# Kernel tuning notes

Measured on AMD Instinct MI355X. Metric: run time of the kernel, lower is better.

## Reference

```python
import jax, jax.numpy as jnp
import numpy as np

BS, SL, N_AGENTS, OBS_DIM, STATE_DIM, N_EDGES, HID = 32, 512, 32, 96, 1024, 64, 256


def _hgcn(w_line, x, H):
    # x: [B, n, 1]; H: [B, n, E]. Faithful to torch HGCN:
    # A = D^{-1/2} H |W| B^{-1} H^T D^{-1/2}, with D, B built from detached H/|W|,
    # inf entries (from 0^{-1} / 0^{-0.5}) zeroed. Diagonal matmuls are implicit scalings.
    w_abs = jnp.abs(w_line)
    Hd = jax.lax.stop_gradient(H)
    d = jnp.einsum('bne,e->bn', Hd, jax.lax.stop_gradient(w_abs))  # [B, n]
    d_is = jnp.where(d > 0, jax.lax.rsqrt(jnp.where(d > 0, d, 1.0)), 0.0)
    b = jnp.sum(Hd, axis=-2)  # [B, E]
    b_inv = jnp.where(b > 0, 1.0 / jnp.where(b > 0, b, 1.0), 0.0)
    t = d_is[..., None] * x                       # D^{-1/2} x
    s = jnp.einsum('bne,bnk->bek', H, t)          # H^T (...)
    s = s * (w_abs[None, :] * b_inv)[..., None]   # |W| B^{-1} (diagonals commute)
    y = jnp.einsum('bne,bek->bnk', H, s)          # H (...)
    return d_is[..., None] * y                    # D^{-1/2} (...)


def _mlp(x, w1, b1, w2, b2):
    return jax.nn.relu(x @ w1 + b1) @ w2 + b2


def setup_inputs() -> dict:
    key = jax.random.key(0)
    ks = jax.random.split(key, 24)
    f = jax.random.normal
    inp = {
        'agent_qs': f(ks[0], (BS, SL, N_AGENTS), jnp.float32),
        'states': f(ks[1], (BS, SL, STATE_DIM), jnp.float32),
        'indiv_us': f(ks[2], (BS, SL, N_AGENTS, OBS_DIM), jnp.float32),
        'edge_W': f(ks[3], (OBS_DIM, N_EDGES), jnp.float32) * 0.1,
        'edge_b': f(ks[4], (N_EDGES,), jnp.float32) * 0.1,
        'wline1': 1.0 + 0.1 * f(ks[5], (N_EDGES,), jnp.float32),
        'wline2': 1.0 + 0.1 * f(ks[6], (N_EDGES,), jnp.float32),
    }
    names = ['hw1', 'hc1', 'hw', 'hc']
    outs = [N_AGENTS, N_AGENTS, N_AGENTS, 1]
    for i, (nm, od) in enumerate(zip(names, outs)):
        inp[nm + '_w1'] = f(ks[7 + 4 * i], (STATE_DIM, HID), jnp.float32) * 0.05
        inp[nm + '_b1'] = f(ks[8 + 4 * i], (HID,), jnp.float32) * 0.05
        inp[nm + '_w2'] = f(ks[9 + 4 * i], (HID, od), jnp.float32) * 0.05
        inp[nm + '_b2'] = f(ks[10 + 4 * i], (od,), jnp.float32) * 0.05
    return inp


def reference(agent_qs, states, indiv_us, edge_W, edge_b, wline1, wline2,
              hw1_w1, hw1_b1, hw1_w2, hw1_b2, hc1_w1, hc1_b1, hc1_w2, hc1_b2,
              hw_w1, hw_b1, hw_w2, hw_b2, hc_w1, hc_b1, hc_w2, hc_b2):
    bs, sl, n = agent_qs.shape
    q = agent_qs.reshape(-1, n)                               # [B, n]
    u = indiv_us.reshape(-1, n, indiv_us.shape[-1])           # [B, n, obs]
    s = states.reshape(-1, states.shape[-1])                  # [B, state_dim]
    H = jax.nn.relu(u @ edge_W + edge_b)                      # hyper_edge_net -> [B, n, E]
    x = q[..., None]                                          # node_features [B, n, 1]
    qs_tot = _hgcn(wline2, _hgcn(wline1, x, H), H)[..., 0]    # two stacked HGCN encoders
    w1 = jnp.abs(_mlp(s, hw1_w1, hw1_b1, hw1_w2, hw1_b2))
    c1 = _mlp(s, hc1_w1, hc1_b1, hc1_w2, hc1_b2)
    qt = jax.nn.elu(qs_tot * w1 + c1)
    w = jnp.abs(_mlp(s, hw_w1, hw_b1, hw_w2, hw_b2))
    c = _mlp(s, hc_w1, hc_b1, hc_w2, hc_b2)[..., 0]
    q_tot = jnp.sum(qt * w, axis=-1) + c
    return q_tot.reshape(bs, sl, 1)
```

## Files before the change

kernel.cpp:

```cpp
#include <hip/hip_runtime.h>
#include <cstdint>

typedef _Float16 f16;
typedef _Float16 f16x2 __attribute__((ext_vector_type(2)));
typedef _Float16 f16x4 __attribute__((ext_vector_type(4)));
typedef _Float16 f16x8 __attribute__((ext_vector_type(8)));
typedef float f32x4 __attribute__((ext_vector_type(4)));

#define AS1U const __attribute__((address_space(1))) unsigned int
#define AS3U __attribute__((address_space(3))) unsigned int

__device__ __forceinline__ void gload_lds16(const void* g, void* l) {
    __builtin_amdgcn_global_load_lds((AS1U*)g, (AS3U*)l, 16, 0, 0);
}

#define WSYNC() asm volatile("s_waitcnt lgkmcnt(0)" ::: "memory")
#define CFENCE() asm volatile("" ::: "memory")

#define BATCH 16384
#define NAG   32
#define OBS   96
#define SDIM  1024
#define NE    64
#define HIDN  256
#define NH    1024

#define NB_ST 1024
#define NB_PW 256
#define NB_SM 101
#define NB_FRONT (NB_ST + NB_PW + NB_SM)

__global__ __launch_bounds__(256) void k_front(
    const float* __restrict__ states,
    const float* __restrict__ w1a, const float* __restrict__ w1b,
    const float* __restrict__ w1c, const float* __restrict__ w1d,
    const float* __restrict__ b1a, const float* __restrict__ b1b,
    const float* __restrict__ b1c, const float* __restrict__ b1d,
    const float* __restrict__ w2a, const float* __restrict__ w2b,
    const float* __restrict__ w2c, const float* __restrict__ w2d,
    f16* __restrict__ states16, f16* __restrict__ W1t, float* __restrict__ b1cat,
    f16* __restrict__ W2t, f16* __restrict__ hcw2) {
    __shared__ float tile[64 * 65];
    const int tid = threadIdx.x;
    int bid = blockIdx.x;

    if (bid < NB_ST) {
        int i = bid * 256 + tid;
        const int n4 = BATCH * SDIM / 4;
        const int stride = NB_ST * 256;
        for (; i < n4; i += stride) {
            float4 v = ((const float4*)states)[i];
            f16x4 h = { (f16)v.x, (f16)v.y, (f16)v.z, (f16)v.w };
            ((f16x4*)states16)[i] = h;
        }
        return;
    }
    bid -= NB_ST;
    if (bid < NB_PW) {
        int mlp = bid >> 6, rem = bid & 63, kt = rem >> 2, ct = rem & 3;
        const float* src = (mlp == 0) ? w1a : (mlp == 1) ? w1b : (mlp == 2) ? w1c : w1d;
        int k0 = kt * 64, c0 = ct * 64;
        for (int i = tid; i < 4096; i += 256) {
            int kk = i >> 6, cc = i & 63;
            tile[kk * 65 + cc] = src[(size_t)(k0 + kk) * 256 + c0 + cc];
        }
        __syncthreads();
        for (int i = tid; i < 4096; i += 256) {
            int cc = i >> 6, kk = i & 63;
            W1t[(size_t)(mlp * 256 + c0 + cc) * 1024 + k0 + kk] = (f16)tile[kk * 65 + cc];
        }
        return;
    }
    bid -= NB_PW;
    {
        int i = bid * 256 + tid;
        if (i < 24576) {
            int mp = i >> 13, rem = i & 8191, oo = rem >> 8, kk = rem & 255;
            const float* src = (mp == 0) ? w2a : (mp == 1) ? w2b : w2c;
            W2t[i] = (f16)src[kk * 32 + oo];
        } else if (i < 24832) {
            int k = i - 24576;
            hcw2[k] = (f16)w2d[k];
        } else if (i < 25856) {
            int n = i - 24832;
            int mlp = n >> 8, c = n & 255;
            const float* bsrc = (mlp == 0) ? b1a : (mlp == 1) ? b1b : (mlp == 2) ? b1c : b1d;
            b1cat[n] = bsrc[c];
        }
    }
}

__global__ __launch_bounds__(512) void k_gemm(
    const f16* __restrict__ A, const f16* __restrict__ B,
    const float* __restrict__ b1cat, const f16* __restrict__ W2t,
    const f16* __restrict__ hcw2, float* __restrict__ Pp) {
    __shared__ __align__(16) char smem[131072];
    f16* Asb = (f16*)smem;
    f16* Bsb = (f16*)(smem + 65536);
    f16* Ts  = (f16*)smem;

    const int tid = threadIdx.x;
    const int w = tid >> 6, l = tid & 63;
    const int lm = l & 15, lk = l >> 4;
    const int wm = w >> 2, wn = w & 3;
    const int p = blockIdx.x;
    const int xcd = p & 7, s = p >> 3;
    const int mt = xcd * 8 + (s >> 2);
    const int nt = s & 3;
    const int m0 = mt * 256, n0 = nt * 256;
    const int c0 = w * 4;
    const int srow = l >> 3;
    const int gchunk = (l & 7) ^ srow;

    float bj[4];
    #pragma unroll
    for (int j = 0; j < 4; j++) bj[j] = b1cat[n0 + wn * 64 + j * 16 + lm];

    f32x4 acc[8][4];
    #pragma unroll
    for (int i = 0; i < 8; i++)
        #pragma unroll
        for (int j = 0; j < 4; j++) acc[i][j] = (f32x4){0.f, 0.f, 0.f, 0.f};

#define STAGE(KT, BI)                                                                     \
    {                                                                                     \
        f16* Ad = Asb + (BI) * 16384;                                                     \
        f16* Bd = Bsb + (BI) * 16384;                                                     \
        _Pragma("unroll")                                                                 \
        for (int i_ = 0; i_ < 4; i_++) {                                                  \
            int cc = c0 + i_;                                                             \
            gload_lds16(&A[(size_t)(m0 + cc * 8 + srow) * 1024 + (KT) * 64 + gchunk * 8], \
                        &Ad[cc * 512]);                                                   \
            gload_lds16(&B[(size_t)(n0 + cc * 8 + srow) * 1024 + (KT) * 64 + gchunk * 8], \
                        &Bd[cc * 512]);                                                   \
        }                                                                                 \
    }

    STAGE(0, 0);
    STAGE(1, 1);

    for (int kt = 0; kt < 16; kt++) {
        if (kt < 15) { asm volatile("s_waitcnt vmcnt(8)" ::: "memory"); }
        else         { asm volatile("s_waitcnt vmcnt(0)" ::: "memory"); }
        CFENCE(); __builtin_amdgcn_s_barrier(); CFENCE();

        const f16* As_ = Asb + (kt & 1) * 16384;
        const f16* Bs_ = Bsb + (kt & 1) * 16384;
        __builtin_amdgcn_s_setprio(1);
        #pragma unroll
        for (int ks = 0; ks < 2; ks++) {
            const int sw = (((ks * 4 + lk) ^ (lm & 7)) << 3);
            f16x8 af[8], bf[4];
            #pragma unroll
            for (int i = 0; i < 8; i++)
                af[i] = *(const f16x8*)&As_[(wm * 128 + i * 16 + lm) * 64 + sw];
            #pragma unroll
            for (int j = 0; j < 4; j++)
                bf[j] = *(const f16x8*)&Bs_[(wn * 64 + j * 16 + lm) * 64 + sw];
            #pragma unroll
            for (int i = 0; i < 8; i++)
                #pragma unroll
                for (int j = 0; j < 4; j++)
                    acc[i][j] = __builtin_amdgcn_mfma_f32_16x16x32_f16(af[i], bf[j], acc[i][j], 0, 0, 0);
        }
        __builtin_amdgcn_s_setprio(0);

        CFENCE(); __builtin_amdgcn_s_barrier(); CFENCE();
        if (kt < 14) STAGE(kt + 2, kt & 1);
    }
#undef STAGE

    const int mlp = nt;
    #pragma unroll
    for (int pass = 0; pass < 2; pass++) {
        if (wm == pass) {
            #pragma unroll
            for (int i = 0; i < 8; i++)
                #pragma unroll
                for (int r = 0; r < 4; r++) {
                    int rl = i * 16 + lk * 4 + r;
                    #pragma unroll
                    for (int j = 0; j < 4; j++) {
                        float v = acc[i][j][r] + bj[j];
                        Ts[rl * 264 + wn * 64 + j * 16 + lm] = (f16)(v > 0.f ? v : 0.f);
                    }
                }
        }
        __syncthreads();
        const int grow = m0 + pass * 128 + w * 16;
        if (mlp < 3) {
            const f16* wb = W2t + mlp * 8192;
            f32x4 acc2[2];
            acc2[0] = (f32x4){0, 0, 0, 0}; acc2[1] = (f32x4){0, 0, 0, 0};
            #pragma unroll
            for (int ks = 0; ks < 8; ks++) {
                f16x8 a  = *(const f16x8*)&Ts[(w * 16 + lm) * 264 + ks * 32 + lk * 8];
                f16x8 b0 = *(const f16x8*)&wb[lm * 256 + ks * 32 + lk * 8];
                f16x8 b1 = *(const f16x8*)&wb[(16 + lm) * 256 + ks * 32 + lk * 8];
                acc2[0] = __builtin_amdgcn_mfma_f32_16x16x32_f16(a, b0, acc2[0], 0, 0, 0);
                acc2[1] = __builtin_amdgcn_mfma_f32_16x16x32_f16(a, b1, acc2[1], 0, 0, 0);
            }
            #pragma unroll
            for (int j2 = 0; j2 < 2; j2++)
                #pragma unroll
                for (int r = 0; r < 4; r++)
                    Pp[(size_t)(grow + lk * 4 + r) * 104 + mlp * 32 + j2 * 16 + lm] = acc2[j2][r];
        } else {
            f32x4 acc2 = (f32x4){0, 0, 0, 0};
            #pragma unroll
            for (int ks = 0; ks < 8; ks++) {
                f16x8 a = *(const f16x8*)&Ts[(w * 16 + lm) * 264 + ks * 32 + lk * 8];
                f16x8 bz = (f16x8){0, 0, 0, 0, 0, 0, 0, 0};
                if (lm == 0) bz = *(const f16x8*)&hcw2[ks * 32 + lk * 8];
                acc2 = __builtin_amdgcn_mfma_f32_16x16x32_f16(a, bz, acc2, 0, 0, 0);
            }
            if (lm == 0)
                #pragma unroll
                for (int r = 0; r < 4; r++)
                    Pp[(size_t)(grow + lk * 4 + r) * 104 + 96] = acc2[r];
        }
        if (pass == 0) __syncthreads();
    }
}

__global__ __launch_bounds__(256) void k_hgcn_ep(
    const float* __restrict__ agent_qs, const float* __restrict__ indiv_us,
    const float* __restrict__ edge_W, const float* __restrict__ edge_b,
    const float* __restrict__ wline1, const float* __restrict__ wline2,
    const float* __restrict__ Pp,
    const float* __restrict__ hw1_b2, const float* __restrict__ hc1_b2,
    const float* __restrict__ hw_b2, const float* __restrict__ hc_b2,
    float* __restrict__ out) {
    __shared__ __align__(16) char arena[34304];
    f16*   eWs   = (f16*)arena;
    float* swa   = (float*)(arena + 13312);
    f16*   HsB   = (f16*)(arena + 13824);
    float* svB   = (float*)(arena + 30720);
    float* sttB  = (float*)(arena + 31744);
    float* sdisB = (float*)(arena + 32256);
    float* sbinvB= (float*)(arena + 33280);

    const int tid = threadIdx.x;
    const int w = tid >> 6, l = tid & 63;
    const int b = blockIdx.x * 4 + w;
    f16*   Hw    = HsB + w * (32 * 66);
    float* sv    = svB + w * 64;
    float* stt   = sttB + w * 32;
    float* sdis  = sdisB + w * 64;
    float* sbinv = sbinvB + w * 64;

    const int nn = l & 31, half = l >> 5;

    float pa0 = 0.f, pc0 = 0.f, pw0 = 0.f;
    float p96a = 0.f, bw1 = 0.f, bc1 = 0.f, bww = 0.f, bhc = 0.f;
    if (half == 0) {
        const float* p0 = Pp + (size_t)b * 104;
        pa0 = p0[nn];
        pc0 = p0[32 + nn];
        pw0 = p0[64 + nn];
        p96a = p0[96];
        bw1 = hw1_b2[nn];  bc1 = hc1_b2[nn];
        bww = hw_b2[nn];   bhc = hc_b2[0];
    }
    float q = agent_qs[(size_t)b * 32 + nn];

    for (int i = tid; i < 6144; i += 256) {
        int k = i >> 6, n = i & 63;
        eWs[n * 104 + k] = (f16)edge_W[i];
    }
    if (tid < 64) swa[tid] = fabsf(wline1[tid]);
    else if (tid < 128) swa[tid] = fabsf(wline2[tid - 64]);
    __syncthreads();

    const int lm = l & 15, lk = l >> 4;
    const float* ub = indiv_us + (size_t)b * (NAG * OBS);

    #pragma unroll
    for (int mt = 0; mt < 2; mt++) {
        f16x8 af[3];
        #pragma unroll
        for (int ks = 0; ks < 3; ks++) {
            const float* up = ub + (mt * 16 + lm) * 96 + ks * 32 + lk * 8;
            float4 v0 = *(const float4*)up;
            float4 v1 = *(const float4*)(up + 4);
            af[ks] = (f16x8){ (f16)v0.x, (f16)v0.y, (f16)v0.z, (f16)v0.w,
                              (f16)v1.x, (f16)v1.y, (f16)v1.z, (f16)v1.w };
        }
        #pragma unroll
        for (int nt = 0; nt < 4; nt++) {
            f32x4 acc = {0.f, 0.f, 0.f, 0.f};
            #pragma unroll
            for (int ks = 0; ks < 3; ks++) {
                f16x8 bb = *(const f16x8*)&eWs[(nt * 16 + lm) * 104 + ks * 32 + lk * 8];
                acc = __builtin_amdgcn_mfma_f32_16x16x32_f16(af[ks], bb, acc, 0, 0, 0);
            }
            int col = nt * 16 + lm;
            float bias = edge_b[col];
            #pragma unroll
            for (int r = 0; r < 4; r++) {
                int row = mt * 16 + lk * 4 + r;
                float hv = acc[r] + bias;
                Hw[row * 66 + col] = (f16)(hv > 0.f ? hv : 0.f);
            }
        }
    }
    WSYNC();

    float bsum = 0.f;
    #pragma unroll
    for (int n = 0; n < 32; n++) bsum += (float)Hw[n * 66 + l];
    sbinv[l] = bsum > 0.f ? 1.f / bsum : 0.f;

    float dd = 0.f;
    #pragma unroll 8
    for (int e2 = 0; e2 < 32; e2++) {
        f16x2 h2 = *(const f16x2*)&Hw[nn * 66 + e2 * 2];
        dd += (float)h2.x * swa[half * 64 + e2 * 2] + (float)h2.y * swa[half * 64 + e2 * 2 + 1];
    }
    float dis = dd > 0.f ? rsqrtf(dd) : 0.f;
    sdis[l] = dis;
    if (half == 0) stt[nn] = dis * q;
    WSYNC();

    float s1 = 0.f;
    #pragma unroll
    for (int n = 0; n < 32; n++) s1 += (float)Hw[n * 66 + l] * stt[n];
    sv[l] = s1 * swa[l] * sbinv[l];
    WSYNC();

    float y1 = 0.f;
    #pragma unroll 8
    for (int e2 = 0; e2 < 32; e2++) {
        f16x2 h2 = *(const f16x2*)&Hw[nn * 66 + e2 * 2];
        y1 += (float)h2.x * sv[e2 * 2] + (float)h2.y * sv[e2 * 2 + 1];
    }
    float x2 = sdis[nn] * y1;
    if (half == 0) stt[nn] = sdis[32 + nn] * x2;
    WSYNC();

    float s2 = 0.f;
    #pragma unroll
    for (int n = 0; n < 32; n++) s2 += (float)Hw[n * 66 + l] * stt[n];
    sv[l] = s2 * swa[64 + l] * sbinv[l];
    WSYNC();

    float y2 = 0.f;
    #pragma unroll 8
    for (int e2 = 0; e2 < 32; e2++) {
        f16x2 h2 = *(const f16x2*)&Hw[nn * 66 + e2 * 2];
        y2 += (float)h2.x * sv[e2 * 2] + (float)h2.y * sv[e2 * 2 + 1];
    }

    float qsv = sdis[32 + nn] * y2;
    float w1v = fabsf(pa0 + bw1);
    float c1v = pc0 + bc1;
    float wwv = fabsf(pw0 + bww);
    float z = qsv * w1v + c1v;
    float qt = z > 0.f ? z : expm1f(z);
    float val = (half == 0) ? qt * wwv : 0.f;
    val += __shfl_xor(val, 1, 32);
    val += __shfl_xor(val, 2, 32);
    val += __shfl_xor(val, 4, 32);
    val += __shfl_xor(val, 8, 32);
    val += __shfl_xor(val, 16, 32);
    if (l == 0) out[b] = val + p96a + bhc;
}

extern "C" void kernel_launch(void* const* d_in, const int* in_sizes, int n_in,
                              void* d_out, int out_size, void* d_ws, size_t ws_size,
                              hipStream_t stream) {
    const float* agent_qs = (const float*)d_in[0];
    const float* states   = (const float*)d_in[1];
    const float* indiv_us = (const float*)d_in[2];
    const float* edge_W   = (const float*)d_in[3];
    const float* edge_b   = (const float*)d_in[4];
    const float* wline1   = (const float*)d_in[5];
    const float* wline2   = (const float*)d_in[6];
    const float* hw1_w1 = (const float*)d_in[7];
    const float* hw1_b1 = (const float*)d_in[8];
    const float* hw1_w2 = (const float*)d_in[9];
    const float* hw1_b2 = (const float*)d_in[10];
    const float* hc1_w1 = (const float*)d_in[11];
    const float* hc1_b1 = (const float*)d_in[12];
    const float* hc1_w2 = (const float*)d_in[13];
    const float* hc1_b2 = (const float*)d_in[14];
    const float* hw_w1  = (const float*)d_in[15];
    const float* hw_b1  = (const float*)d_in[16];
    const float* hw_w2  = (const float*)d_in[17];
    const float* hw_b2  = (const float*)d_in[18];
    const float* hc_w1  = (const float*)d_in[19];
    const float* hc_b1  = (const float*)d_in[20];
    const float* hc_w2  = (const float*)d_in[21];
    const float* hc_b2  = (const float*)d_in[22];

    char* ws = (char*)d_ws;
    size_t o_states16 = 0;
    size_t o_W1t  = o_states16 + (size_t)BATCH * SDIM * 2;
    size_t o_b1   = o_W1t + (size_t)NH * SDIM * 2;
    size_t o_W2t  = o_b1 + 4096;
    size_t o_hcw2 = o_W2t + 49152;
    size_t o_Pp   = o_hcw2 + 512;

    f16*   states16 = (f16*)(ws + o_states16);
    f16*   W1t      = (f16*)(ws + o_W1t);
    float* b1cat    = (float*)(ws + o_b1);
    f16*   W2t      = (f16*)(ws + o_W2t);
    f16*   hcw2     = (f16*)(ws + o_hcw2);
    float* Pp       = (float*)(ws + o_Pp);

    k_front<<<NB_FRONT, 256, 0, stream>>>(
        states,
        hw1_w1, hc1_w1, hw_w1, hc_w1, hw1_b1, hc1_b1, hw_b1, hc_b1,
        hw1_w2, hc1_w2, hw_w2, hc_w2,
        states16, W1t, b1cat, W2t, hcw2);
    k_gemm<<<256, 512, 0, stream>>>(states16, W1t, b1cat, W2t, hcw2, Pp);
    k_hgcn_ep<<<BATCH / 4, 256, 0, stream>>>(
        agent_qs, indiv_us, edge_W, edge_b, wline1, wline2, Pp,
        hw1_b2, hc1_b2, hw_b2, hc_b2, (float*)d_out);
}
```

Baseline: 120.6 us.

## Split GEMM k-tile into four quadrant phases interleaving LDS reads with MFMA

Restructures the inner k-tile loop of the fp16 MFMA GEMM into four quadrant sub-phases (A rows 0-3/4-7 × B cols 0-1/2-3). Each phase loads only the fragments it needs, with barriers between phases, so LDS reads overlap with MFMA work from other waves and register pressure drops. The next-tile global-to-LDS staging is issued before the last quadrant's MFMAs so it overlaps compute. It adds more barriers per k-tile and a trailing __syncthreads, which may cost synchronization overhead.

Result: no change. 120.4 us (-0.2%).

```diff
diff --git a/kernel.cpp b/kernel.cpp
--- a/kernel.cpp
+++ b/kernel.cpp
@@ -146,29 +146,78 @@
 
         const f16* As_ = Asb + (kt & 1) * 16384;
         const f16* Bs_ = Bsb + (kt & 1) * 16384;
+        const int swlo = ((lk ^ (lm & 7)) << 3);
+        const int swhi = (((4 + lk) ^ (lm & 7)) << 3);
+
+        f16x8 af[4][2], bf01[2][2], bf23[2][2];
+
+        #pragma unroll
+        for (int i = 0; i < 4; i++) {
+            af[i][0] = *(const f16x8*)&As_[(wm * 128 + i * 16 + lm) * 64 + swlo];
+            af[i][1] = *(const f16x8*)&As_[(wm * 128 + i * 16 + lm) * 64 + swhi];
+        }
+        #pragma unroll
+        for (int j = 0; j < 2; j++) {
+            bf01[j][0] = *(const f16x8*)&Bs_[(wn * 64 + j * 16 + lm) * 64 + swlo];
+            bf01[j][1] = *(const f16x8*)&Bs_[(wn * 64 + j * 16 + lm) * 64 + swhi];
+        }
         __builtin_amdgcn_s_setprio(1);
         #pragma unroll
-        for (int ks = 0; ks < 2; ks++) {
-            const int sw = (((ks * 4 + lk) ^ (lm & 7)) << 3);
-            f16x8 af[8], bf[4];
-            #pragma unroll
-            for (int i = 0; i < 8; i++)
-                af[i] = *(const f16x8*)&As_[(wm * 128 + i * 16 + lm) * 64 + sw];
-            #pragma unroll
-            for (int j = 0; j < 4; j++)
-                bf[j] = *(const f16x8*)&Bs_[(wn * 64 + j * 16 + lm) * 64 + sw];
-            #pragma unroll
-            for (int i = 0; i < 8; i++)
-                #pragma unroll
-                for (int j = 0; j < 4; j++)
-                    acc[i][j] = __builtin_amdgcn_mfma_f32_16x16x32_f16(af[i], bf[j], acc[i][j], 0, 0, 0);
-        }
+        for (int ks = 0; ks < 2; ks++)
+            #pragma unroll
+            for (int i = 0; i < 4; i++)
+                #pragma unroll
+                for (int j = 0; j < 2; j++)
+                    acc[i][j] = __builtin_amdgcn_mfma_f32_16x16x32_f16(af[i][ks], bf01[j][ks], acc[i][j], 0, 0, 0);
         __builtin_amdgcn_s_setprio(0);
-
         CFENCE(); __builtin_amdgcn_s_barrier(); CFENCE();
+
+        #pragma unroll
+        for (int j = 0; j < 2; j++) {
+            bf23[j][0] = *(const f16x8*)&Bs_[(wn * 64 + (2 + j) * 16 + lm) * 64 + swlo];
+            bf23[j][1] = *(const f16x8*)&Bs_[(wn * 64 + (2 + j) * 16 + lm) * 64 + swhi];
+        }
+        __builtin_amdgcn_s_setprio(1);
+        #pragma unroll
+        for (int ks = 0; ks < 2; ks++)
+            #pragma unroll
+            for (int i = 0; i < 4; i++)
+                #pragma unroll
+                for (int j = 0; j < 2; j++)
+                    acc[i][2 + j] = __builtin_amdgcn_mfma_f32_16x16x32_f16(af[i][ks], bf23[j][ks], acc[i][2 + j], 0, 0, 0);
+        __builtin_amdgcn_s_setprio(0);
+        CFENCE(); __builtin_amdgcn_s_barrier(); CFENCE();
+
+        #pragma unroll
+        for (int i = 0; i < 4; i++) {
+            af[i][0] = *(const f16x8*)&As_[(wm * 128 + (4 + i) * 16 + lm) * 64 + swlo];
+            af[i][1] = *(const f16x8*)&As_[(wm * 128 + (4 + i) * 16 + lm) * 64 + swhi];
+        }
+        __builtin_amdgcn_s_setprio(1);
+        #pragma unroll
+        for (int ks = 0; ks < 2; ks++)
+            #pragma unroll
+            for (int i = 0; i < 4; i++)
+                #pragma unroll
+                for (int j = 0; j < 2; j++)
+                    acc[4 + i][j] = __builtin_amdgcn_mfma_f32_16x16x32_f16(af[i][ks], bf01[j][ks], acc[4 + i][j], 0, 0, 0);
+        __builtin_amdgcn_s_setprio(0);
+        CFENCE(); __builtin_amdgcn_s_barrier(); CFENCE();
+
         if (kt < 14) STAGE(kt + 2, kt & 1);
+        __builtin_amdgcn_s_setprio(1);
+        #pragma unroll
+        for (int ks = 0; ks < 2; ks++)
+            #pragma unroll
+            for (int i = 0; i < 4; i++)
+                #pragma unroll
+                for (int j = 0; j < 2; j++)
+                    acc[4 + i][2 + j] = __builtin_amdgcn_mfma_f32_16x16x32_f16(af[i][ks], bf23[j][ks], acc[4 + i][2 + j], 0, 0, 0);
+        __builtin_amdgcn_s_setprio(0);
     }
 #undef STAGE
+
+    __syncthreads();
 
     const int mlp = nt;
     #pragma unroll
```
